# Performance work log

Measured on AMD Instinct MI355X. Metric: run time of the kernel, lower is better.

The kernel has to match this reference:

```python
import jax, jax.numpy as jnp
import numpy as np

N_EMBD = 768
N_HEAD = 12
HEAD_DIM = N_EMBD // N_HEAD


def setup_inputs() -> dict:
    key = jax.random.key(0)
    ks = jax.random.split(key, 9)
    s = 0.02
    return {
        "x": jax.random.normal(ks[0], (2, 4096, N_EMBD), dtype=jnp.float32),
        "Wq": jax.random.normal(ks[1], (N_EMBD, N_EMBD), dtype=jnp.float32) * s,
        "bq": jnp.zeros((N_EMBD,), dtype=jnp.float32),
        "Wk": jax.random.normal(ks[2], (N_EMBD, N_EMBD), dtype=jnp.float32) * s,
        "bk": jnp.zeros((N_EMBD,), dtype=jnp.float32),
        "Wv": jax.random.normal(ks[3], (N_EMBD, N_EMBD), dtype=jnp.float32) * s,
        "bv": jnp.zeros((N_EMBD,), dtype=jnp.float32),
        "Wo": jax.random.normal(ks[4], (N_EMBD, N_EMBD), dtype=jnp.float32) * s,
        "bo": jnp.zeros((N_EMBD,), dtype=jnp.float32),
    }


def reference(x, Wq, bq, Wk, bk, Wv, bv, Wo, bo):
    B, T, C = x.shape
    H, D = N_HEAD, HEAD_DIM
    # torch Linear: y = x @ W.T + b
    q = (x @ Wq.T + bq).reshape(B, T, H, D).transpose(0, 2, 1, 3)  # [B,H,T,D]
    k = (x @ Wk.T + bk).reshape(B, T, H, D).transpose(0, 2, 1, 3)
    v = (x @ Wv.T + bv).reshape(B, T, H, D).transpose(0, 2, 1, 3)
    scale = 1.0 / jnp.sqrt(jnp.float32(D))
    att = jnp.einsum("bhqd,bhkd->bhqk", q, k) * scale  # [B,H,T,T]
    causal = jnp.tril(jnp.ones((T, T), dtype=bool))
    att = jnp.where(causal[None, None], att, -jnp.inf)
    att = jax.nn.softmax(att, axis=-1)
    y = jnp.einsum("bhqk,bhkd->bhqd", att, v)
    y = y.transpose(0, 2, 1, 3).reshape(B, T, C)
    return y @ Wo.T + bo
```

## Files before the change

### kernel.cpp

```cpp
#include <hip/hip_runtime.h>

typedef __bf16 bf16_t;
typedef __bf16 bf16x4 __attribute__((ext_vector_type(4)));
typedef __bf16 bf16x8 __attribute__((ext_vector_type(8)));
typedef float  f32x4  __attribute__((ext_vector_type(4)));
typedef float  f32x16 __attribute__((ext_vector_type(16)));
typedef unsigned int u32;

#define MFMA16(a, b, c) __builtin_amdgcn_mfma_f32_16x16x32_bf16((a), (b), (c), 0, 0, 0)
#define MFMA32(a, b, c) __builtin_amdgcn_mfma_f32_32x32x16_bf16((a), (b), (c), 0, 0, 0)

__device__ __forceinline__ void gld_lds16(const bf16_t* g, bf16_t* l) {
  __builtin_amdgcn_global_load_lds((__attribute__((address_space(1))) void*)g,
                                   (__attribute__((address_space(3))) void*)l, 16, 0, 0);
}
__device__ __forceinline__ u32 cvt_pk_bf16(float lo, float hi) {
  u32 r;
  asm("v_cvt_pk_bf16_f32 %0, %1, %2" : "=v"(r) : "v"(lo), "v"(hi));
  return r;
}

__global__ void cast_f32_bf16(const float* __restrict__ s, bf16_t* __restrict__ d, int n) {
  int i = (blockIdx.x * blockDim.x + threadIdx.x) * 4;
  if (i >= n) return;
  float4 v = *(const float4*)(s + i);
  bf16x4 o;
  o[0] = (bf16_t)v.x; o[1] = (bf16_t)v.y; o[2] = (bf16_t)v.z; o[3] = (bf16_t)v.w;
  *(bf16x4*)(d + i) = o;
}

__global__ void prep_w(const float* __restrict__ Wq, const float* __restrict__ Wk,
                       const float* __restrict__ Wv, const float* __restrict__ Wo,
                       const float* __restrict__ bq, const float* __restrict__ bk,
                       const float* __restrict__ bv,
                       bf16_t* __restrict__ wqkv, bf16_t* __restrict__ wob,
                       float* __restrict__ qkvb) {
  const int NW = 768 * 768;
  const int t = blockIdx.x * 256 + threadIdx.x;
  const int i = t * 4;
  if (i < 3 * NW) {
    const float* s; int off;
    if (i < NW)          { s = Wq; off = i; }
    else if (i < 2 * NW) { s = Wk; off = i - NW; }
    else                 { s = Wv; off = i - 2 * NW; }
    float4 v = *(const float4*)(s + off);
    bf16x4 o;
    o[0] = (bf16_t)v.x; o[1] = (bf16_t)v.y; o[2] = (bf16_t)v.z; o[3] = (bf16_t)v.w;
    *(bf16x4*)(wqkv + i) = o;
  } else if (i < 4 * NW) {
    const int off = i - 3 * NW;
    float4 v = *(const float4*)(Wo + off);
    bf16x4 o;
    o[0] = (bf16_t)v.x; o[1] = (bf16_t)v.y; o[2] = (bf16_t)v.z; o[3] = (bf16_t)v.w;
    *(bf16x4*)(wob + off) = o;
  }
  if (t < 2304) qkvb[t] = t < 768 ? bq[t] : (t < 1536 ? bk[t - 768] : bv[t - 1536]);
}

__global__ __launch_bounds__(256) void gemm_qkv(
    const bf16_t* __restrict__ A, const bf16_t* __restrict__ B,
    const float* __restrict__ bias,
    bf16_t* __restrict__ qb, bf16_t* __restrict__ kb2, bf16_t* __restrict__ vtb) {
  __shared__ __align__(16) bf16_t As[128 * 64];
  __shared__ __align__(16) bf16_t Bs[128 * 64];
  const int K = 768;
  const int p = blockIdx.x;
  const int xcd = p & 7, u = p >> 3;
  const int bm = xcd * 8 + u / 18;
  const int bn = u - (u / 18) * 18;
  const int tid = threadIdx.x;
  const int w = tid >> 6, l = tid & 63, lg = l >> 4, ln = l & 15;
  const int wr = w >> 1, wc = w & 1;
  const int lr8 = l >> 3, lc8 = l & 7;
  const int region = (bn * 128) / 768;
  const int ln7 = ln & 7;
  f32x4 acc[4][4] = {};
  for (int kb = 0; kb < K / 64; ++kb) {
    const int k0 = kb * 64;
#pragma unroll
    for (int i = 0; i < 4; ++i) {
      const int row = w * 32 + i * 8 + lr8;
      const int so = k0 + ((lc8 ^ (row & 7)) << 3);
      gld_lds16(A + (size_t)(bm * 128 + row) * K + so, As + (w * 32 + i * 8) * 64 + l * 8);
      gld_lds16(B + (size_t)(bn * 128 + row) * K + so, Bs + (w * 32 + i * 8) * 64 + l * 8);
    }
    __syncthreads();
#pragma unroll
    for (int kk = 0; kk < 2; ++kk) {
      bf16x8 af[4], bfr[4];
#pragma unroll
      for (int m = 0; m < 4; ++m) {
        const int jc = ((kk * 4 + lg) ^ ln7) << 3;
        af[m]  = *(const bf16x8*)(As + (wr * 64 + m * 16 + ln) * 64 + jc);
        bfr[m] = *(const bf16x8*)(Bs + (wc * 64 + m * 16 + ln) * 64 + jc);
      }
      if (region != 2) {
#pragma unroll
        for (int m = 0; m < 4; ++m)
#pragma unroll
          for (int n = 0; n < 4; ++n) acc[m][n] = MFMA16(af[m], bfr[n], acc[m][n]);
      } else {
#pragma unroll
        for (int m = 0; m < 4; ++m)
#pragma unroll
          for (int n = 0; n < 4; ++n) acc[m][n] = MFMA16(bfr[n], af[m], acc[m][n]);
      }
    }
    __syncthreads();
  }
  if (region != 2) {
    const float scl = (region == 0) ? 0.18033688011112042f : 1.0f;
    bf16_t* dst = region == 0 ? qb : kb2;
#pragma unroll
    for (int m = 0; m < 4; ++m)
#pragma unroll
      for (int n = 0; n < 4; ++n)
#pragma unroll
        for (int j = 0; j < 4; ++j) {
          const int gm = bm * 128 + wr * 64 + m * 16 + lg * 4 + j;
          const int gn = bn * 128 + wc * 64 + n * 16 + ln;
          const float v = (acc[m][n][j] + bias[gn]) * scl;
          const int c = gn - region * 768;
          const int bb = gm >> 12, tt = gm & 4095;
          const int hh = c >> 6, d = c & 63;
          dst[((size_t)(bb * 12 + hh) * 4096 + tt) * 64 + d] = (bf16_t)v;
        }
  } else {
#pragma unroll
    for (int m = 0; m < 4; ++m)
#pragma unroll
      for (int n = 0; n < 4; ++n)
#pragma unroll
        for (int j = 0; j < 4; ++j) {
          const int gn = bn * 128 + wc * 64 + n * 16 + lg * 4 + j;
          const int gm = bm * 128 + wr * 64 + m * 16 + ln;
          const float v = acc[m][n][j] + bias[gn];
          const int c = gn - 1536;
          const int bb = gm >> 12, tt = gm & 4095;
          const int hh = c >> 6, d = c & 63;
          vtb[((size_t)(bb * 12 + hh) * 64 + d) * 4096 + tt] = (bf16_t)v;
        }
  }
}

__global__ __launch_bounds__(512) void attn_fwd(
    const bf16_t* __restrict__ q, const bf16_t* __restrict__ k,
    const bf16_t* __restrict__ vt, bf16_t* __restrict__ y) {
  __shared__ __align__(16) unsigned char SMEM[65536];
  bf16_t* Ks = (bf16_t*)SMEM;
  bf16_t* Vs = (bf16_t*)(SMEM + 32768);
  float*  osh = (float*)SMEM;
  float*  lsh = (float*)(SMEM + 32768);

  const int p = blockIdx.x;
  const int xcd = p & 7, slot = p >> 3;
  const int hb = xcd + 8 * (slot % 3);
  const int qt = 31 - slot / 3;
  const int tid = threadIdx.x;
  const int w = tid >> 6, l = tid & 63, lq = l & 31, lh = l >> 5;
  const int wq = w >> 1, wc = w & 1;
  const size_t hbo = (size_t)hb * (4096 * 64);
  const bf16_t* qh = q + hbo;
  const bf16_t* kh = k + hbo;
  const bf16_t* vh = vt + hbo;

  const int q0 = qt * 128 + wq * 32;
  const int qidx = q0 + lq;
  const int nst = qt + 1;

  const int sr = ((tid >> 8) << 5) | (tid & 31);
  const int sc = ((((tid >> 6) & 3) << 1) | ((tid >> 5) & 1)) << 3;
  const bf16_t* k0src = kh + ((size_t)sr * 64 + sc);
  const bf16_t* k1src = k0src + 4096;
  const bf16_t* v0src = vh + ((size_t)sr * 4096 + sc);
  const bf16_t* v1src = v0src + 64;

  bf16x8 qf[4];
#pragma unroll
  for (int ds = 0; ds < 4; ++ds)
    qf[ds] = *(const bf16x8*)(qh + (size_t)qidx * 64 + 16 * ds + 8 * lh);
  bf16x8 ones;
#pragma unroll
  for (int j = 0; j < 8; ++j) ones[j] = (bf16_t)1.0f;

  gld_lds16(k0src, Ks + tid * 8);
  gld_lds16(k1src, Ks + 4096 + tid * 8);
  gld_lds16(v0src, Vs + tid * 8);
  gld_lds16(v1src, Vs + 4096 + tid * 8);
  __syncthreads();

  f32x16 o0 = {}, o1 = {}, osum = {};

  int cur = 0;
  for (int i = 0; i < nst; ++i) {
    if (i + 1 < nst) {
      bf16_t* kd = Ks + (cur ^ 1) * 8192;
      bf16_t* vd = Vs + (cur ^ 1) * 8192;
      gld_lds16(k0src + 8192, kd + tid * 8);
      gld_lds16(k1src + 8192, kd + 4096 + tid * 8);
      gld_lds16(v0src + 128, vd + tid * 8);
      gld_lds16(v1src + 128, vd + 4096 + tid * 8);
    }
    k0src += 8192; k1src += 8192; v0src += 128; v1src += 128;
    const int t = 2 * i + wc;
    if (t * 64 <= q0 + 31) {
      const int kvb = t * 64;
      const bool diag = (kvb + 63 > q0);
      const bf16_t* KsW = Ks + (cur * 2 + wc) * 4096;
      const bf16_t* VsW = Vs + (cur * 2 + wc) * 4096;
      u32 pq[2][8];
#pragma unroll
      for (int kb = 0; kb < 2; ++kb) {
        f32x16 st = {};
        __builtin_amdgcn_s_setprio(1);
#pragma unroll
        for (int ds = 0; ds < 4; ++ds) {
          bf16x8 kf = *(const bf16x8*)(KsW + (kb * 4 + ds) * 512 + l * 8);
          st = MFMA32(kf, qf[ds], st);
        }
        __builtin_amdgcn_s_setprio(0);
        float pv[16];
#pragma unroll
        for (int r = 0; r < 16; ++r) pv[r] = __builtin_amdgcn_exp2f(st[r]);
        if (diag) {
          const int kb0 = kvb + kb * 32 + 4 * lh;
#pragma unroll
          for (int r = 0; r < 16; ++r)
            if (kb0 + (r & 3) + 8 * (r >> 2) > qidx) pv[r] = 0.f;
        }
#pragma unroll
        for (int g = 0; g < 8; ++g) pq[kb][g] = cvt_pk_bf16(pv[2 * g], pv[2 * g + 1]);
#pragma unroll
        for (int ks2 = 0; ks2 < 2; ++ks2) {
          asm("v_permlane32_swap_b32 %0, %1" : "+v"(pq[kb][4 * ks2 + 0]), "+v"(pq[kb][4 * ks2 + 2]));
          asm("v_permlane32_swap_b32 %0, %1" : "+v"(pq[kb][4 * ks2 + 1]), "+v"(pq[kb][4 * ks2 + 3]));
        }
      }
      __builtin_amdgcn_s_setprio(1);
#pragma unroll
      for (int ks = 0; ks < 4; ++ks) {
        bf16x8 pa = *(const bf16x8*)&pq[ks >> 1][(ks & 1) * 4];
        bf16x8 v0 = *(const bf16x8*)(VsW + ks * 512 + l * 8);
        bf16x8 v1 = *(const bf16x8*)(VsW + (4 + ks) * 512 + l * 8);
        o0 = MFMA32(pa, v0, o0);
        o1 = MFMA32(pa, v1, o1);
        osum = MFMA32(pa, ones, osum);
      }
      __builtin_amdgcn_s_setprio(0);
    }
    __syncthreads();
    cur ^= 1;
  }

  if (wc == 1) {
#pragma unroll
    for (int r = 0; r < 16; ++r) {
      osh[wq * 2048 + r * 64 + l] = o0[r];
      osh[wq * 2048 + (16 + r) * 64 + l] = o1[r];
    }
    if (lq == 0) {
#pragma unroll
      for (int r = 0; r < 16; ++r)
        lsh[wq * 32 + (r & 3) + 8 * (r >> 2) + 4 * lh] = osum[r];
    }
  }
  __syncthreads();
  if (wc == 0) {
#pragma unroll
    for (int r = 0; r < 16; ++r) {
      o0[r] += osh[wq * 2048 + r * 64 + l];
      o1[r] += osh[wq * 2048 + (16 + r) * 64 + l];
    }
    float linv[16];
#pragma unroll
    for (int r = 0; r < 16; ++r) {
      const int rl = (r & 3) + 8 * (r >> 2) + 4 * lh;
      linv[r] = 1.0f / (osum[r] + lsh[wq * 32 + rl]);
    }
    const int b = hb / 12, h = hb - b * 12;
#pragma unroll
    for (int r = 0; r < 16; ++r) {
      const int row = q0 + (r & 3) + 8 * (r >> 2) + 4 * lh;
      bf16_t* yr = y + ((size_t)b * 4096 + row) * 768 + h * 64 + lq;
      yr[0]  = (bf16_t)(o0[r] * linv[r]);
      yr[32] = (bf16_t)(o1[r] * linv[r]);
    }
  }
}

__global__ __launch_bounds__(256) void gemm_out(
    const bf16_t* __restrict__ A, const bf16_t* __restrict__ B,
    const float* __restrict__ bias, float* __restrict__ out) {
  __shared__ __align__(16) bf16_t As[128 * 64];
  __shared__ __align__(16) bf16_t Bs[128 * 64];
  const int K = 768;
  const int p = blockIdx.x;
  const int xcd = p & 7, u = p >> 3;
  const int bm = xcd * 8 + u / 6;
  const int bn = u - (u / 6) * 6;
  const int tid = threadIdx.x;
  const int w = tid >> 6, l = tid & 63, lg = l >> 4, ln = l & 15;
  const int wr = w >> 1, wc = w & 1;
  const int lr8 = l >> 3, lc8 = l & 7;
  const int ln7 = ln & 7;
  f32x4 acc[4][4] = {};
  for (int kb = 0; kb < K / 64; ++kb) {
    const int k0 = kb * 64;
#pragma unroll
    for (int i = 0; i < 4; ++i) {
      const int row = w * 32 + i * 8 + lr8;
      const int so = k0 + ((lc8 ^ (row & 7)) << 3);
      gld_lds16(A + (size_t)(bm * 128 + row) * K + so, As + (w * 32 + i * 8) * 64 + l * 8);
      gld_lds16(B + (size_t)(bn * 128 + row) * K + so, Bs + (w * 32 + i * 8) * 64 + l * 8);
    }
    __syncthreads();
#pragma unroll
    for (int kk = 0; kk < 2; ++kk) {
      bf16x8 af[4], bfr[4];
#pragma unroll
      for (int m = 0; m < 4; ++m) {
        const int jc = ((kk * 4 + lg) ^ ln7) << 3;
        af[m]  = *(const bf16x8*)(As + (wr * 64 + m * 16 + ln) * 64 + jc);
        bfr[m] = *(const bf16x8*)(Bs + (wc * 64 + m * 16 + ln) * 64 + jc);
      }
#pragma unroll
      for (int m = 0; m < 4; ++m)
#pragma unroll
        for (int n = 0; n < 4; ++n) acc[m][n] = MFMA16(af[m], bfr[n], acc[m][n]);
    }
    __syncthreads();
  }
  const int gn0 = bn * 128 + wc * 64;
#pragma unroll
  for (int m = 0; m < 4; ++m) {
#pragma unroll
    for (int n = 0; n < 4; ++n) {
#pragma unroll
      for (int j = 0; j < 4; ++j) {
        const int gm = bm * 128 + wr * 64 + m * 16 + lg * 4 + j;
        const int gn = gn0 + n * 16 + ln;
        out[(size_t)gm * 768 + gn] = acc[m][n][j] + bias[gn];
      }
    }
  }
}

extern "C" void kernel_launch(void* const* d_in, const int* in_sizes, int n_in,
                              void* d_out, int out_size, void* d_ws, size_t ws_size,
                              hipStream_t stream) {
  const float* x  = (const float*)d_in[0];
  const float* Wq = (const float*)d_in[1];
  const float* bq = (const float*)d_in[2];
  const float* Wk = (const float*)d_in[3];
  const float* bk = (const float*)d_in[4];
  const float* Wv = (const float*)d_in[5];
  const float* bv = (const float*)d_in[6];
  const float* Wo = (const float*)d_in[7];
  const float* bo = (const float*)d_in[8];
  float* out = (float*)d_out;

  const int M = 8192, C = 768, QKV = 2304;
  bf16_t* xb   = (bf16_t*)d_ws;
  bf16_t* wqkv = xb + (size_t)M * C;
  bf16_t* wob  = wqkv + (size_t)QKV * C;
  float*  qkvb = (float*)(wob + (size_t)C * C);
  bf16_t* qbuf = (bf16_t*)(qkvb + QKV);
  bf16_t* kbuf = qbuf + (size_t)M * C;
  bf16_t* vtb  = kbuf + (size_t)M * C;
  bf16_t* yb   = xb;

  cast_f32_bf16<<<6144, 256, 0, stream>>>(x, xb, M * C);
  prep_w<<<2304, 256, 0, stream>>>(Wq, Wk, Wv, Wo, bq, bk, bv, wqkv, wob, qkvb);

  gemm_qkv<<<1152, 256, 0, stream>>>(xb, wqkv, qkvb, qbuf, kbuf, vtb);
  attn_fwd<<<768, 512, 0, stream>>>(qbuf, kbuf, vtb, yb);
  gemm_out<<<384, 256, 0, stream>>>(yb, wob, bo, out);
}
```

Baseline: 177.6 us.

## Split each 64-key tile across wave pairs instead of alternating whole tiles

The attention kernel now streams 64-key KV tiles, one per iteration, instead of 128-key tiles, and has the two column waves split each tile into 32-key halves. The old scheme gave each wave its own whole 64-key tile. LDS use falls from 64 KB to about 33 KB, which could allow more resident blocks per CU and better balances work on the diagonal tiles. The cost is twice as many loop iterations and barriers, and each wave issues smaller MFMA batches per step.

```diff
diff --git a/kernel.cpp b/kernel.cpp
--- a/kernel.cpp
+++ b/kernel.cpp
@@ -146,9 +146,9 @@
 __global__ __launch_bounds__(512) void attn_fwd(
     const bf16_t* __restrict__ q, const bf16_t* __restrict__ k,
     const bf16_t* __restrict__ vt, bf16_t* __restrict__ y) {
-  __shared__ __align__(16) unsigned char SMEM[65536];
+  __shared__ __align__(16) unsigned char SMEM[33280];
   bf16_t* Ks = (bf16_t*)SMEM;
-  bf16_t* Vs = (bf16_t*)(SMEM + 32768);
+  bf16_t* Vs = (bf16_t*)(SMEM + 16384);
   float*  osh = (float*)SMEM;
   float*  lsh = (float*)(SMEM + 32768);
 
@@ -166,14 +166,12 @@
 
   const int q0 = qt * 128 + wq * 32;
   const int qidx = q0 + lq;
-  const int nst = qt + 1;
+  const int nst = 2 * qt + 2;
 
   const int sr = ((tid >> 8) << 5) | (tid & 31);
   const int sc = ((((tid >> 6) & 3) << 1) | ((tid >> 5) & 1)) << 3;
-  const bf16_t* k0src = kh + ((size_t)sr * 64 + sc);
-  const bf16_t* k1src = k0src + 4096;
-  const bf16_t* v0src = vh + ((size_t)sr * 4096 + sc);
-  const bf16_t* v1src = v0src + 64;
+  const bf16_t* ksrc = kh + ((size_t)sr * 64 + sc);
+  const bf16_t* vsrc = vh + ((size_t)sr * 4096 + sc);
 
   bf16x8 qf[4];
 #pragma unroll
@@ -183,65 +181,55 @@
 #pragma unroll
   for (int j = 0; j < 8; ++j) ones[j] = (bf16_t)1.0f;
 
-  gld_lds16(k0src, Ks + tid * 8);
-  gld_lds16(k1src, Ks + 4096 + tid * 8);
-  gld_lds16(v0src, Vs + tid * 8);
-  gld_lds16(v1src, Vs + 4096 + tid * 8);
+  gld_lds16(ksrc, Ks + tid * 8);
+  gld_lds16(vsrc, Vs + tid * 8);
   __syncthreads();
 
   f32x16 o0 = {}, o1 = {}, osum = {};
 
   int cur = 0;
-  for (int i = 0; i < nst; ++i) {
-    if (i + 1 < nst) {
-      bf16_t* kd = Ks + (cur ^ 1) * 8192;
-      bf16_t* vd = Vs + (cur ^ 1) * 8192;
-      gld_lds16(k0src + 8192, kd + tid * 8);
-      gld_lds16(k1src + 8192, kd + 4096 + tid * 8);
-      gld_lds16(v0src + 128, vd + tid * 8);
-      gld_lds16(v1src + 128, vd + 4096 + tid * 8);
-    }
-    k0src += 8192; k1src += 8192; v0src += 128; v1src += 128;
-    const int t = 2 * i + wc;
-    if (t * 64 <= q0 + 31) {
-      const int kvb = t * 64;
+  for (int t = 0; t < nst; ++t) {
+    if (t + 1 < nst) {
+      gld_lds16(ksrc + 4096, Ks + (cur ^ 1) * 4096 + tid * 8);
+      gld_lds16(vsrc + 64, Vs + (cur ^ 1) * 4096 + tid * 8);
+    }
+    ksrc += 4096; vsrc += 64;
+    const int kvb = t * 64;
+    if (kvb <= q0 + 31) {
       const bool diag = (kvb + 63 > q0);
-      const bf16_t* KsW = Ks + (cur * 2 + wc) * 4096;
-      const bf16_t* VsW = Vs + (cur * 2 + wc) * 4096;
-      u32 pq[2][8];
-#pragma unroll
-      for (int kb = 0; kb < 2; ++kb) {
-        f32x16 st = {};
-        __builtin_amdgcn_s_setprio(1);
-#pragma unroll
-        for (int ds = 0; ds < 4; ++ds) {
-          bf16x8 kf = *(const bf16x8*)(KsW + (kb * 4 + ds) * 512 + l * 8);
-          st = MFMA32(kf, qf[ds], st);
-        }
-        __builtin_amdgcn_s_setprio(0);
-        float pv[16];
-#pragma unroll
-        for (int r = 0; r < 16; ++r) pv[r] = __builtin_amdgcn_exp2f(st[r]);
-        if (diag) {
-          const int kb0 = kvb + kb * 32 + 4 * lh;
-#pragma unroll
-          for (int r = 0; r < 16; ++r)
-            if (kb0 + (r & 3) + 8 * (r >> 2) > qidx) pv[r] = 0.f;
-        }
-#pragma unroll
-        for (int g = 0; g < 8; ++g) pq[kb][g] = cvt_pk_bf16(pv[2 * g], pv[2 * g + 1]);
-#pragma unroll
-        for (int ks2 = 0; ks2 < 2; ++ks2) {
-          asm("v_permlane32_swap_b32 %0, %1" : "+v"(pq[kb][4 * ks2 + 0]), "+v"(pq[kb][4 * ks2 + 2]));
-          asm("v_permlane32_swap_b32 %0, %1" : "+v"(pq[kb][4 * ks2 + 1]), "+v"(pq[kb][4 * ks2 + 3]));
-        }
-      }
+      const bf16_t* KsW = Ks + cur * 4096;
+      const bf16_t* VsW = Vs + cur * 4096;
+      f32x16 st = {};
       __builtin_amdgcn_s_setprio(1);
 #pragma unroll
-      for (int ks = 0; ks < 4; ++ks) {
-        bf16x8 pa = *(const bf16x8*)&pq[ks >> 1][(ks & 1) * 4];
-        bf16x8 v0 = *(const bf16x8*)(VsW + ks * 512 + l * 8);
-        bf16x8 v1 = *(const bf16x8*)(VsW + (4 + ks) * 512 + l * 8);
+      for (int ds = 0; ds < 4; ++ds) {
+        bf16x8 kf = *(const bf16x8*)(KsW + (wc * 4 + ds) * 512 + l * 8);
+        st = MFMA32(kf, qf[ds], st);
+      }
+      __builtin_amdgcn_s_setprio(0);
+      float pv[16];
+#pragma unroll
+      for (int r = 0; r < 16; ++r) pv[r] = __builtin_amdgcn_exp2f(st[r]);
+      if (diag) {
+        const int kb0 = kvb + wc * 32 + 4 * lh;
+#pragma unroll
+        for (int r = 0; r < 16; ++r)
+          if (kb0 + (r & 3) + 8 * (r >> 2) > qidx) pv[r] = 0.f;
+      }
+      u32 pq[8];
+#pragma unroll
+      for (int g = 0; g < 8; ++g) pq[g] = cvt_pk_bf16(pv[2 * g], pv[2 * g + 1]);
+#pragma unroll
+      for (int ks2 = 0; ks2 < 2; ++ks2) {
+        asm("v_permlane32_swap_b32 %0, %1" : "+v"(pq[4 * ks2 + 0]), "+v"(pq[4 * ks2 + 2]));
+        asm("v_permlane32_swap_b32 %0, %1" : "+v"(pq[4 * ks2 + 1]), "+v"(pq[4 * ks2 + 3]));
+      }
+      __builtin_amdgcn_s_setprio(1);
+#pragma unroll
+      for (int ks = 0; ks < 2; ++ks) {
+        bf16x8 pa = *(const bf16x8*)&pq[ks * 4];
+        bf16x8 v0 = *(const bf16x8*)(VsW + (2 * wc + ks) * 512 + l * 8);
+        bf16x8 v1 = *(const bf16x8*)(VsW + (4 + 2 * wc + ks) * 512 + l * 8);
         o0 = MFMA32(pa, v0, o0);
         o1 = MFMA32(pa, v1, o1);
         osum = MFMA32(pa, ones, osum);
```

Measured after the change: 171.7 us. 1.03x faster.
